# Optimization experiments

Measured on AMD Instinct MI355X. Metric: run time of the kernel, lower is better.

The kernel has to match this reference:

```python
import jax, jax.numpy as jnp
import numpy as np

B, S, D = 8, 4096, 512
H, DH = 8, 64  # heads, dim_head; inner_dim = H*DH = 512
EPS = 1e-6


def setup_inputs() -> dict:
    key = jax.random.key(0)
    ks = jax.random.split(key, 9)
    scale = 1.0 / np.sqrt(D)
    inner = H * DH
    return {
        "x": jax.random.normal(ks[0], (B, S, D), dtype=jnp.float32),
        "Wq": jax.random.normal(ks[1], (D, inner), dtype=jnp.float32) * scale,
        "bq": jax.random.normal(ks[2], (inner,), dtype=jnp.float32) * 0.01,
        "Wk": jax.random.normal(ks[3], (D, inner), dtype=jnp.float32) * scale,
        "bk": jax.random.normal(ks[4], (inner,), dtype=jnp.float32) * 0.01,
        "Wv": jax.random.normal(ks[5], (D, inner), dtype=jnp.float32) * scale,
        "bv": jax.random.normal(ks[6], (inner,), dtype=jnp.float32) * 0.01,
        "Wo": jax.random.normal(ks[7], (inner, D), dtype=jnp.float32) * (1.0 / np.sqrt(inner)),
        "bo": jax.random.normal(ks[8], (D,), dtype=jnp.float32) * 0.01,
    }


def _phi(x):
    # elu(x) + 1, the fast-transformers default feature map
    return jax.nn.elu(x) + 1.0


def reference(x, Wq, bq, Wk, bk, Wv, bv, Wo, bo):
    b, s, _ = x.shape
    q = (x @ Wq + bq).reshape(b, s, H, DH)
    k = (x @ Wk + bk).reshape(b, s, H, DH)
    v = (x @ Wv + bv).reshape(b, s, H, DH)

    Qf = _phi(q)  # [b, s, h, d]
    Kf = _phi(k)  # [b, s, h, d]

    # KV = sum_s Kf_s (outer) v_s  -> [b, h, d, m]
    KV = jnp.einsum('bshd,bshm->bhdm', Kf, v)
    # normalizer: Z = 1 / (Qf . sum_s Kf + eps)  -> [b, s, h]
    Ksum = Kf.sum(axis=1)  # [b, h, d]
    Z = 1.0 / (jnp.einsum('bshd,bhd->bsh', Qf, Ksum) + EPS)
    out = jnp.einsum('bshd,bhdm,bsh->bshm', Qf, KV, Z)  # [b, s, h, m]

    out = out.reshape(b, s, H * DH)
    return out @ Wo + bo  # dropout is identity at inference
```

## Files before the change

kernel.cpp:

```cpp
#include <hip/hip_runtime.h>
#include <hip/hip_fp16.h>


constexpr int Ss = 4096;
constexpr int Dd = 512;
constexpr int Hh = 8;
constexpr int Mtot = 8 * 4096;
constexpr float EPSF = 1e-6f;

typedef short v8s __attribute__((ext_vector_type(8)));
typedef float v4f __attribute__((ext_vector_type(4)));

__device__ __forceinline__ short f2bf(float f) {
  unsigned u = __float_as_uint(f);
  u += 0x7fff + ((u >> 16) & 1);
  return (short)(u >> 16);
}
__device__ __forceinline__ float bf2f(short s) {
  return __uint_as_float(((unsigned)(unsigned short)s) << 16);
}
__device__ __forceinline__ void async_cp16(const void* g, void* l) {
  __builtin_amdgcn_global_load_lds((__attribute__((address_space(1))) void*)g,
                                   (__attribute__((address_space(3))) void*)l, 16, 0, 0);
}

__global__ __launch_bounds__(256) void prep_w(
    const float* __restrict__ W0, const float* __restrict__ W1,
    const float* __restrict__ W2, const float* __restrict__ W3,
    short* __restrict__ Th, short* __restrict__ Tl)
{
  const float* W = (blockIdx.z == 0) ? W0 : (blockIdx.z == 1) ? W1
                  : (blockIdx.z == 2) ? W2 : W3;
  short* th = Th + (size_t)blockIdx.z * 512 * 512;
  short* tl = Tl + (size_t)blockIdx.z * 512 * 512;
  __shared__ float tile[32][33];
  const int t = threadIdx.x;
  const int tx = t & 31, ty = t >> 5;
  const int k0 = blockIdx.x * 32, n0 = blockIdx.y * 32;
#pragma unroll
  for (int r = 0; r < 32; r += 8)
    tile[ty + r][tx] = W[(size_t)(k0 + ty + r) * 512 + n0 + tx];
  __syncthreads();
#pragma unroll
  for (int r = 0; r < 32; r += 8) {
    const float v = tile[tx][ty + r];
    const short h = f2bf(v);
    const short l = f2bf(v - bf2f(h));
    th[(size_t)(n0 + ty + r) * 512 + k0 + tx] = h;
    tl[(size_t)(n0 + ty + r) * 512 + k0 + tx] = l;
  }
}

__global__ __launch_bounds__(256) void split_x(
    const float* __restrict__ X, short* __restrict__ H, short* __restrict__ L, int n4)
{
  const int i = blockIdx.x * 256 + threadIdx.x;
  if (i >= n4) return;
  const float4 x = reinterpret_cast<const float4*>(X)[i];
  short4 h, l;
  h.x = f2bf(x.x); l.x = f2bf(x.x - bf2f(h.x));
  h.y = f2bf(x.y); l.y = f2bf(x.y - bf2f(h.y));
  h.z = f2bf(x.z); l.z = f2bf(x.z - bf2f(h.z));
  h.w = f2bf(x.w); l.w = f2bf(x.w - bf2f(h.w));
  reinterpret_cast<short4*>(H)[i] = h;
  reinterpret_cast<short4*>(L)[i] = l;
}

__device__ __forceinline__ void stage_tile(
    const short* __restrict__ pA, const short* __restrict__ pB,
    short* as, short* bs, int k0, int t)
{
#pragma unroll
  for (int c = 0; c < 2; ++c) {
    const int idx = t + c * 512;
    const int row = idx >> 2;
    const int q = (idx & 3) ^ ((row >> 1) & 3);
    const size_t g = (size_t)row * 512 + k0 + q * 8;
    async_cp16(pA + g, as + idx * 8);
    async_cp16(pB + g, bs + idx * 8);
  }
}

__global__ __launch_bounds__(512, 2) void gemm_qkv(
    const short* __restrict__ Ah, const short* __restrict__ Al,
    const short* __restrict__ Wth, const short* __restrict__ Wtl,
    const float* __restrict__ bq, const float* __restrict__ bk,
    const float* __restrict__ bv,
    __half* __restrict__ Qf, __half* __restrict__ Kf, __half* __restrict__ Vv)
{
  __shared__ short As[2][256 * 32];
  __shared__ short Bs[2][256 * 32];

  const int mat = blockIdx.y >> 1;
  const int col0 = (blockIdx.y & 1) * 256;
  const int row0 = blockIdx.x * 256;
  const float* bias = (mat == 0) ? bq : (mat == 1) ? bk : bv;
  __half* Co = (mat == 0) ? Qf : (mat == 1) ? Kf : Vv;
  const int act = (mat < 2);

  const short* Ahb = Ah + (size_t)row0 * 512;
  const short* Alb = Al + (size_t)row0 * 512;
  const short* Bhb = Wth + (size_t)mat * 512 * 512 + (size_t)col0 * 512;
  const short* Blb = Wtl + (size_t)mat * 512 * 512 + (size_t)col0 * 512;

  const int t = threadIdx.x;
  const int lane = t & 63;
  const int wv = t >> 6;
  const int wm = wv >> 2, wn = wv & 3;
  const int mr = lane & 15, kq = lane >> 4;

  int a_off[8], b_off[4];
#pragma unroll
  for (int i = 0; i < 8; ++i) {
    const int ma = wm * 128 + i * 16 + mr;
    a_off[i] = ma * 32 + (kq ^ ((ma >> 1) & 3)) * 8;
  }
#pragma unroll
  for (int j = 0; j < 4; ++j) {
    const int nb = wn * 64 + j * 16 + mr;
    b_off[j] = nb * 32 + (kq ^ ((nb >> 1) & 3)) * 8;
  }

  v4f acc[8][4];
#pragma unroll
  for (int i = 0; i < 8; ++i)
#pragma unroll
    for (int j = 0; j < 4; ++j) acc[i][j] = (v4f){0.f, 0.f, 0.f, 0.f};

  stage_tile(Ahb, Bhb, As[0], Bs[0], 0, t);

  for (int kt = 0; kt < 48; ++kt) {
    const int cur = kt & 1;
    if (kt + 1 < 48) {
      const int nx = kt + 1;
      const int pass = nx >> 4;
      const short* pA = (pass == 2) ? Alb : Ahb;
      const short* pB = (pass == 1) ? Blb : Bhb;
      stage_tile(pA, pB, As[cur ^ 1], Bs[cur ^ 1], (nx & 15) * 32, t);
      asm volatile("s_waitcnt vmcnt(4)" ::: "memory");
    } else {
      asm volatile("s_waitcnt vmcnt(0)" ::: "memory");
    }
    __builtin_amdgcn_s_barrier();
    asm volatile("" ::: "memory");

    v8s fb[4];
#pragma unroll
    for (int j = 0; j < 4; ++j)
      fb[j] = *reinterpret_cast<const v8s*>(&Bs[cur][b_off[j]]);
    __builtin_amdgcn_s_setprio(1);
#pragma unroll
    for (int i = 0; i < 8; ++i) {
      const v8s fa = *reinterpret_cast<const v8s*>(&As[cur][a_off[i]]);
#pragma unroll
      for (int j = 0; j < 4; ++j)
        acc[i][j] = __builtin_amdgcn_mfma_f32_16x16x32_bf16(fa, fb[j], acc[i][j], 0, 0, 0);
    }
    __builtin_amdgcn_s_setprio(0);
    asm volatile("" ::: "memory");
    __builtin_amdgcn_s_barrier();
  }

#pragma unroll
  for (int j = 0; j < 4; ++j) {
    const int nc = col0 + wn * 64 + j * 16 + mr;
    const float bz = bias[nc];
#pragma unroll
    for (int i = 0; i < 8; ++i) {
      const int mbase = row0 + wm * 128 + i * 16 + kq * 4;
#pragma unroll
      for (int r = 0; r < 4; ++r) {
        float v = acc[i][j][r] + bz;
        if (act) v = (v > 0.f) ? (v + 1.f) : __expf(v);
        Co[(size_t)(mbase + r) * 512 + nc] = __float2half(v);
      }
    }
  }
}

__global__ __launch_bounds__(512, 2) void gemm_split(
    const short* __restrict__ Ah, const short* __restrict__ Al,
    const short* __restrict__ Bh, const short* __restrict__ Bl,
    const float* __restrict__ bias, float* __restrict__ Cf)
{
  __shared__ short As[2][256 * 32];
  __shared__ short Bs[2][256 * 32];

  const int col0 = blockIdx.y * 256;
  const int row0 = blockIdx.x * 256;

  const short* Ahb = Ah + (size_t)row0 * 512;
  const short* Alb = Al + (size_t)row0 * 512;
  const short* Bhb = Bh + (size_t)col0 * 512;
  const short* Blb = Bl + (size_t)col0 * 512;

  const int t = threadIdx.x;
  const int lane = t & 63;
  const int wv = t >> 6;
  const int wm = wv >> 2, wn = wv & 3;
  const int mr = lane & 15, kq = lane >> 4;

  int a_off[8], b_off[4];
#pragma unroll
  for (int i = 0; i < 8; ++i) {
    const int ma = wm * 128 + i * 16 + mr;
    a_off[i] = ma * 32 + (kq ^ ((ma >> 1) & 3)) * 8;
  }
#pragma unroll
  for (int j = 0; j < 4; ++j) {
    const int nb = wn * 64 + j * 16 + mr;
    b_off[j] = nb * 32 + (kq ^ ((nb >> 1) & 3)) * 8;
  }

  v4f acc[8][4];
#pragma unroll
  for (int i = 0; i < 8; ++i)
#pragma unroll
    for (int j = 0; j < 4; ++j) acc[i][j] = (v4f){0.f, 0.f, 0.f, 0.f};

  stage_tile(Ahb, Bhb, As[0], Bs[0], 0, t);

  for (int kt = 0; kt < 48; ++kt) {
    const int cur = kt & 1;
    if (kt + 1 < 48) {
      const int nx = kt + 1;
      const int pass = nx >> 4;
      const short* pA = (pass == 2) ? Alb : Ahb;
      const short* pB = (pass == 1) ? Blb : Bhb;
      stage_tile(pA, pB, As[cur ^ 1], Bs[cur ^ 1], (nx & 15) * 32, t);
      asm volatile("s_waitcnt vmcnt(4)" ::: "memory");
    } else {
      asm volatile("s_waitcnt vmcnt(0)" ::: "memory");
    }
    __builtin_amdgcn_s_barrier();
    asm volatile("" ::: "memory");

    v8s fb[4];
#pragma unroll
    for (int j = 0; j < 4; ++j)
      fb[j] = *reinterpret_cast<const v8s*>(&Bs[cur][b_off[j]]);
    __builtin_amdgcn_s_setprio(1);
#pragma unroll
    for (int i = 0; i < 8; ++i) {
      const v8s fa = *reinterpret_cast<const v8s*>(&As[cur][a_off[i]]);
#pragma unroll
      for (int j = 0; j < 4; ++j)
        acc[i][j] = __builtin_amdgcn_mfma_f32_16x16x32_bf16(fa, fb[j], acc[i][j], 0, 0, 0);
    }
    __builtin_amdgcn_s_setprio(0);
    asm volatile("" ::: "memory");
    __builtin_amdgcn_s_barrier();
  }

#pragma unroll
  for (int j = 0; j < 4; ++j) {
    const int nc = col0 + wn * 64 + j * 16 + mr;
    const float bz = bias[nc];
#pragma unroll
    for (int i = 0; i < 8; ++i) {
      const int mbase = row0 + wm * 128 + i * 16 + kq * 4;
#pragma unroll
      for (int r = 0; r < 4; ++r) Cf[(size_t)(mbase + r) * 512 + nc] = acc[i][j][r] + bz;
    }
  }
}

__global__ __launch_bounds__(256) void kv_stage1(
    const __half* __restrict__ Kf, const __half* __restrict__ V,
    float* __restrict__ KVp, float* __restrict__ Ksp)
{
  const int sc = blockIdx.x, bh = blockIdx.y;
  const int b = bh >> 3, h = bh & 7;
  __shared__ float Ks[64][68];
  __shared__ float Vs[64][68];
  const int tid = threadIdx.x;
  const int dx = (tid >> 4) * 4;
  const int mx = (tid & 15) * 4;
  float acc[4][4];
#pragma unroll
  for (int i = 0; i < 4; ++i)
#pragma unroll
    for (int j = 0; j < 4; ++j) acc[i][j] = 0.f;
  float ksum_acc = 0.f;
  const size_t base = (size_t)b * Ss * Dd + (size_t)h * 64;

  for (int s0 = sc * 256; s0 < sc * 256 + 256; s0 += 64) {
#pragma unroll
    for (int l = 0; l < 2; ++l) {
      const int idx = tid + l * 256;
      const int rr = idx >> 3, cq = idx & 7;
      const size_t g = base + (size_t)(s0 + rr) * Dd + cq * 8;
      const __half2* k2 = reinterpret_cast<const __half2*>(Kf + g);
      const __half2* v2 = reinterpret_cast<const __half2*>(V + g);
#pragma unroll
      for (int u = 0; u < 4; ++u) {
        const float2 kf = __half22float2(k2[u]);
        const float2 vf = __half22float2(v2[u]);
        Ks[rr][cq * 8 + u * 2] = kf.x; Ks[rr][cq * 8 + u * 2 + 1] = kf.y;
        Vs[rr][cq * 8 + u * 2] = vf.x; Vs[rr][cq * 8 + u * 2 + 1] = vf.y;
      }
    }
    __syncthreads();
#pragma unroll 4
    for (int s = 0; s < 64; ++s) {
      const float4 kd = *reinterpret_cast<const float4*>(&Ks[s][dx]);
      const float4 vm = *reinterpret_cast<const float4*>(&Vs[s][mx]);
      const float ka[4] = {kd.x, kd.y, kd.z, kd.w};
      const float va[4] = {vm.x, vm.y, vm.z, vm.w};
#pragma unroll
      for (int i = 0; i < 4; ++i)
#pragma unroll
        for (int j = 0; j < 4; ++j) acc[i][j] = fmaf(ka[i], va[j], acc[i][j]);
    }
    if (tid < 64) {
#pragma unroll 8
      for (int s = 0; s < 64; ++s) ksum_acc += Ks[s][tid];
    }
    __syncthreads();
  }

  const size_t pb = (size_t)(sc * 64 + bh);
#pragma unroll
  for (int i = 0; i < 4; ++i) {
    const float4 ov = {acc[i][0], acc[i][1], acc[i][2], acc[i][3]};
    *reinterpret_cast<float4*>(&KVp[(pb * 64 + dx + i) * 64 + mx]) = ov;
  }
  if (tid < 64) Ksp[pb * 64 + tid] = ksum_acc;
}

__global__ __launch_bounds__(256) void kv_stage2(
    const float* __restrict__ KVp, const float* __restrict__ Ksp,
    float* __restrict__ KV, float* __restrict__ Ksum)
{
  const int bh = blockIdx.x, t = threadIdx.x;
  for (int e = t; e < 4096; e += 256) {
    float s = 0.f;
#pragma unroll
    for (int sc = 0; sc < 16; ++sc) s += KVp[((size_t)(sc * 64 + bh) << 12) + e];
    KV[(size_t)bh * 4096 + e] = s;
  }
  if (t < 64) {
    float s = 0.f;
#pragma unroll
    for (int sc = 0; sc < 16; ++sc) s += Ksp[(size_t)(sc * 64 + bh) * 64 + t];
    Ksum[bh * 64 + t] = s;
  }
}

__global__ __launch_bounds__(256) void attn_combine(
    const __half* __restrict__ Qf, const float* __restrict__ KV,
    const float* __restrict__ Ksum, short* __restrict__ Oh, short* __restrict__ Ol)
{
  const int h = blockIdx.y;
  const int r0 = blockIdx.x * 64;
  const int b = r0 >> 12;
  const int bh = b * Hh + h;
  __shared__ float Qs[64][68];
  __shared__ float KVs[64][68];
  __shared__ float Ksums[64];
  __shared__ float Zs[64];
  const int tid = threadIdx.x;

#pragma unroll
  for (int l = 0; l < 2; ++l) {
    const int idx = tid + l * 256;
    const int rr = idx >> 3, cq = idx & 7;
    const __half2* q2 = reinterpret_cast<const __half2*>(
        Qf + (size_t)(r0 + rr) * Dd + h * 64 + cq * 8);
#pragma unroll
    for (int u = 0; u < 4; ++u) {
      const float2 qf = __half22float2(q2[u]);
      Qs[rr][cq * 8 + u * 2] = qf.x; Qs[rr][cq * 8 + u * 2 + 1] = qf.y;
    }
  }
#pragma unroll
  for (int l = 0; l < 4; ++l) {
    const int idx = tid + l * 256;
    const int rr = idx >> 4, cq = idx & 15;
    *reinterpret_cast<float4*>(&KVs[rr][cq * 4]) = *reinterpret_cast<const float4*>(
        &KV[(size_t)bh * 4096 + rr * 64 + cq * 4]);
  }
  if (tid < 64) Ksums[tid] = Ksum[bh * 64 + tid];
  __syncthreads();

  if (tid < 64) {
    float z = 0.f;
#pragma unroll 8
    for (int d = 0; d < 64; ++d) z = fmaf(Qs[tid][d], Ksums[d], z);
    Zs[tid] = 1.f / (z + EPSF);
  }
  __syncthreads();

  const int rx = (tid >> 4) * 4, mx = (tid & 15) * 4;
  float acc[4][4];
#pragma unroll
  for (int i = 0; i < 4; ++i)
#pragma unroll
    for (int j = 0; j < 4; ++j) acc[i][j] = 0.f;

#pragma unroll 4
  for (int d = 0; d < 64; ++d) {
    const float4 vm = *reinterpret_cast<const float4*>(&KVs[d][mx]);
    const float va[4] = {vm.x, vm.y, vm.z, vm.w};
#pragma unroll
    for (int i = 0; i < 4; ++i) {
      const float q = Qs[rx + i][d];
#pragma unroll
      for (int j = 0; j < 4; ++j) acc[i][j] = fmaf(q, va[j], acc[i][j]);
    }
  }

#pragma unroll
  for (int i = 0; i < 4; ++i) {
    const float z = Zs[rx + i];
    short4 hv, lv;
    float o;
    o = acc[i][0] * z; hv.x = f2bf(o); lv.x = f2bf(o - bf2f(hv.x));
    o = acc[i][1] * z; hv.y = f2bf(o); lv.y = f2bf(o - bf2f(hv.y));
    o = acc[i][2] * z; hv.z = f2bf(o); lv.z = f2bf(o - bf2f(hv.z));
    o = acc[i][3] * z; hv.w = f2bf(o); lv.w = f2bf(o - bf2f(hv.w));
    const size_t off = (size_t)(r0 + rx + i) * Dd + h * 64 + mx;
    *reinterpret_cast<short4*>(&Oh[off]) = hv;
    *reinterpret_cast<short4*>(&Ol[off]) = lv;
  }
}

extern "C" void kernel_launch(void* const* d_in, const int* in_sizes, int n_in,
                              void* d_out, int out_size, void* d_ws, size_t ws_size,
                              hipStream_t stream) {
  const float* x  = (const float*)d_in[0];
  const float* Wq = (const float*)d_in[1];
  const float* bq = (const float*)d_in[2];
  const float* Wk = (const float*)d_in[3];
  const float* bk = (const float*)d_in[4];
  const float* Wv = (const float*)d_in[5];
  const float* bv = (const float*)d_in[6];
  const float* Wo = (const float*)d_in[7];
  const float* bo = (const float*)d_in[8];
  float* out = (float*)d_out;

  char* ws = (char*)d_ws;
  const size_t MB = (size_t)1 << 20;
  short*  x_hi  = (short*)(ws);
  short*  x_lo  = (short*)(ws + 32 * MB);
  short*  Wt_hi = (short*)(ws + 64 * MB);
  short*  Wt_lo = (short*)(ws + 66 * MB);
  __half* Qf    = (__half*)(ws + 68 * MB);
  __half* Kf    = (__half*)(ws + 100 * MB);
  __half* Vv    = (__half*)(ws + 132 * MB);
  float*  KVp   = (float*)(ws + 164 * MB);
  float*  Ksp   = (float*)(ws + 181 * MB);
  float*  KV    = (float*)(ws + 182 * MB);
  float*  Ksum  = (float*)(ws + 183 * MB);
  short*  attn_hi = x_hi;
  short*  attn_lo = x_lo;
  const size_t WSTEP = (size_t)512 * 512;

  prep_w<<<dim3(16, 16, 4), 256, 0, stream>>>(Wq, Wk, Wv, Wo, Wt_hi, Wt_lo);
  split_x<<<Mtot * Dd / 4 / 256, 256, 0, stream>>>(x, x_hi, x_lo, Mtot * Dd / 4);

  gemm_qkv<<<dim3(Mtot / 256, 6), 512, 0, stream>>>(
      x_hi, x_lo, Wt_hi, Wt_lo, bq, bk, bv, Qf, Kf, Vv);

  kv_stage1<<<dim3(16, 64), 256, 0, stream>>>(Kf, Vv, KVp, Ksp);
  kv_stage2<<<64, 256, 0, stream>>>(KVp, Ksp, KV, Ksum);
  attn_combine<<<dim3(Mtot / 64, Hh), 256, 0, stream>>>(Qf, KV, Ksum, attn_hi, attn_lo);

  gemm_split<<<dim3(Mtot / 256, 2), 512, 0, stream>>>(
      attn_hi, attn_lo, Wt_hi + 3 * WSTEP, Wt_lo + 3 * WSTEP, bo, out);
}
```

Before: 497.9 us.

## Restructure split-bf16 GEMM k-loop into 64-wide tiles with interleaved chunk prefetch

Replaces the per-iteration 32-wide K tile loop in both GEMM kernels with a shared helper that processes 64-wide K tiles (24 iterations instead of 48). Global-to-LDS loads for the next tile are split into four chunks issued between MFMA phases, spreading memory traffic across the compute. The aim is fewer barrier/waitcnt round trips per unit of MFMA work and better overlap of loads with matrix math. It doubles LDS use per block (64 KB), which may limit occupancy at 2 blocks per CU, and adds more barriers inside each iteration.

```diff
diff --git a/kernel.cpp b/kernel.cpp
--- a/kernel.cpp
+++ b/kernel.cpp
@@ -66,18 +66,123 @@
   reinterpret_cast<short4*>(L)[i] = l;
 }
 
-__device__ __forceinline__ void stage_tile(
+__device__ __forceinline__ void stage_chunk(
     const short* __restrict__ pA, const short* __restrict__ pB,
-    short* as, short* bs, int k0, int t)
-{
-#pragma unroll
-  for (int c = 0; c < 2; ++c) {
-    const int idx = t + c * 512;
-    const int row = idx >> 2;
-    const int q = (idx & 3) ^ ((row >> 1) & 3);
-    const size_t g = (size_t)row * 512 + k0 + q * 8;
-    async_cp16(pA + g, as + idx * 8);
-    async_cp16(pB + g, bs + idx * 8);
+    short* asub, short* bsub, int kb, int rh, int t)
+{
+  const int row = rh * 128 + (t >> 2);
+  const int q = t & 3;
+  const int qs = q ^ ((row >> 1) & 3);
+  const size_t g = (size_t)row * 512 + kb + qs * 8;
+  const int d = rh * 4096 + t * 8;
+  async_cp16(pA + g, asub + d);
+  async_cp16(pB + g, bsub + d);
+}
+
+__device__ __forceinline__ void kloop_8ph(
+    const short* __restrict__ Ahb, const short* __restrict__ Alb,
+    const short* __restrict__ Bhb, const short* __restrict__ Blb,
+    short* asb, short* bsb,
+    int wm, int wn, int mr, int kq, int t,
+    v4f (&acc)[8][4])
+{
+  constexpr int NT = 24;
+#pragma unroll
+  for (int i = 0; i < 8; ++i)
+#pragma unroll
+    for (int j = 0; j < 4; ++j) acc[i][j] = (v4f){0.f, 0.f, 0.f, 0.f};
+
+  int a_off[8], b_off[4];
+#pragma unroll
+  for (int i = 0; i < 8; ++i) {
+    const int ma = wm * 128 + i * 16 + mr;
+    a_off[i] = ma * 32 + (kq ^ ((ma >> 1) & 3)) * 8;
+  }
+#pragma unroll
+  for (int j = 0; j < 4; ++j) {
+    const int nb = wn * 64 + j * 16 + mr;
+    b_off[j] = nb * 32 + (kq ^ ((nb >> 1) & 3)) * 8;
+  }
+
+#pragma unroll
+  for (int c = 0; c < 4; ++c)
+    stage_chunk(Ahb, Bhb, asb + (c & 1) * 8192, bsb + (c & 1) * 8192,
+                (c & 1) * 32, c >> 1, t);
+
+  for (int kt = 0; kt < NT; ++kt) {
+    const int cur = kt & 1;
+    const short* as0 = asb + cur * 16384;
+    const short* as1 = as0 + 8192;
+    const short* bs0 = bsb + cur * 16384;
+    const short* bs1 = bs0 + 8192;
+    short* An = asb + (cur ^ 1) * 16384;
+    short* Bn = bsb + (cur ^ 1) * 16384;
+    const int nx = kt + 1;
+    const int pass = nx >> 3;
+    const short* pA = (pass == 2) ? Alb : Ahb;
+    const short* pB = (pass == 1) ? Blb : Bhb;
+    const int kb = (nx & 7) * 64;
+
+    if (nx < NT) {
+      stage_chunk(pA, pB, An, Bn, kb, 0, t);
+      asm volatile("s_waitcnt vmcnt(2)" ::: "memory");
+    } else {
+      asm volatile("s_waitcnt vmcnt(0)" ::: "memory");
+    }
+    __builtin_amdgcn_s_barrier();
+    asm volatile("" ::: "memory");
+
+    v8s fb[4][2];
+#pragma unroll
+    for (int j = 0; j < 4; ++j) {
+      fb[j][0] = *reinterpret_cast<const v8s*>(&bs0[b_off[j]]);
+      fb[j][1] = *reinterpret_cast<const v8s*>(&bs1[b_off[j]]);
+    }
+    {
+      const v8s fa00 = *reinterpret_cast<const v8s*>(&as0[a_off[0]]);
+      const v8s fa01 = *reinterpret_cast<const v8s*>(&as1[a_off[0]]);
+      const v8s fa10 = *reinterpret_cast<const v8s*>(&as0[a_off[1]]);
+      const v8s fa11 = *reinterpret_cast<const v8s*>(&as1[a_off[1]]);
+      __builtin_amdgcn_s_setprio(1);
+#pragma unroll
+      for (int j = 0; j < 4; ++j) {
+        acc[0][j] = __builtin_amdgcn_mfma_f32_16x16x32_bf16(fa00, fb[j][0], acc[0][j], 0, 0, 0);
+        acc[0][j] = __builtin_amdgcn_mfma_f32_16x16x32_bf16(fa01, fb[j][1], acc[0][j], 0, 0, 0);
+        acc[1][j] = __builtin_amdgcn_mfma_f32_16x16x32_bf16(fa10, fb[j][0], acc[1][j], 0, 0, 0);
+        acc[1][j] = __builtin_amdgcn_mfma_f32_16x16x32_bf16(fa11, fb[j][1], acc[1][j], 0, 0, 0);
+      }
+      __builtin_amdgcn_s_setprio(0);
+    }
+    asm volatile("" ::: "memory");
+    __builtin_amdgcn_s_barrier();
+
+#pragma unroll
+    for (int p = 1; p < 4; ++p) {
+      const v8s fa00 = *reinterpret_cast<const v8s*>(&as0[a_off[2 * p]]);
+      const v8s fa01 = *reinterpret_cast<const v8s*>(&as1[a_off[2 * p]]);
+      const v8s fa10 = *reinterpret_cast<const v8s*>(&as0[a_off[2 * p + 1]]);
+      const v8s fa11 = *reinterpret_cast<const v8s*>(&as1[a_off[2 * p + 1]]);
+      if (nx < NT)
+        stage_chunk(pA, pB, An + (p & 1) * 8192, Bn + (p & 1) * 8192,
+                    kb + (p & 1) * 32, p >> 1, t);
+      __builtin_amdgcn_s_barrier();
+      asm volatile("" ::: "memory");
+      __builtin_amdgcn_s_setprio(1);
+#pragma unroll
+      for (int j = 0; j < 4; ++j) {
+        acc[2 * p][j] =
+            __builtin_amdgcn_mfma_f32_16x16x32_bf16(fa00, fb[j][0], acc[2 * p][j], 0, 0, 0);
+        acc[2 * p][j] =
+            __builtin_amdgcn_mfma_f32_16x16x32_bf16(fa01, fb[j][1], acc[2 * p][j], 0, 0, 0);
+        acc[2 * p + 1][j] =
+            __builtin_amdgcn_mfma_f32_16x16x32_bf16(fa10, fb[j][0], acc[2 * p + 1][j], 0, 0, 0);
+        acc[2 * p + 1][j] =
+            __builtin_amdgcn_mfma_f32_16x16x32_bf16(fa11, fb[j][1], acc[2 * p + 1][j], 0, 0, 0);
+      }
+      __builtin_amdgcn_s_setprio(0);
+      asm volatile("" ::: "memory");
+      __builtin_amdgcn_s_barrier();
+    }
   }
 }
 
@@ -88,8 +193,8 @@
     const float* __restrict__ bv,
     __half* __restrict__ Qf, __half* __restrict__ Kf, __half* __restrict__ Vv)
 {
-  __shared__ short As[2][256 * 32];
-  __shared__ short Bs[2][256 * 32];
+  __shared__ __align__(16) short As[2][2][8192];
+  __shared__ __align__(16) short Bs[2][2][8192];
 
   const int mat = blockIdx.y >> 1;
   const int col0 = (blockIdx.y & 1) * 256;
@@ -109,57 +214,8 @@
   const int wm = wv >> 2, wn = wv & 3;
   const int mr = lane & 15, kq = lane >> 4;
 
-  int a_off[8], b_off[4];
-#pragma unroll
-  for (int i = 0; i < 8; ++i) {
-    const int ma = wm * 128 + i * 16 + mr;
-    a_off[i] = ma * 32 + (kq ^ ((ma >> 1) & 3)) * 8;
-  }
-#pragma unroll
-  for (int j = 0; j < 4; ++j) {
-    const int nb = wn * 64 + j * 16 + mr;
-    b_off[j] = nb * 32 + (kq ^ ((nb >> 1) & 3)) * 8;
-  }
-
   v4f acc[8][4];
-#pragma unroll
-  for (int i = 0; i < 8; ++i)
-#pragma unroll
-    for (int j = 0; j < 4; ++j) acc[i][j] = (v4f){0.f, 0.f, 0.f, 0.f};
-
-  stage_tile(Ahb, Bhb, As[0], Bs[0], 0, t);
-
-  for (int kt = 0; kt < 48; ++kt) {
-    const int cur = kt & 1;
-    if (kt + 1 < 48) {
-      const int nx = kt + 1;
-      const int pass = nx >> 4;
-      const short* pA = (pass == 2) ? Alb : Ahb;
-      const short* pB = (pass == 1) ? Blb : Bhb;
-      stage_tile(pA, pB, As[cur ^ 1], Bs[cur ^ 1], (nx & 15) * 32, t);
-      asm volatile("s_waitcnt vmcnt(4)" ::: "memory");
-    } else {
-      asm volatile("s_waitcnt vmcnt(0)" ::: "memory");
-    }
-    __builtin_amdgcn_s_barrier();
-    asm volatile("" ::: "memory");
-
-    v8s fb[4];
-#pragma unroll
-    for (int j = 0; j < 4; ++j)
-      fb[j] = *reinterpret_cast<const v8s*>(&Bs[cur][b_off[j]]);
-    __builtin_amdgcn_s_setprio(1);
-#pragma unroll
-    for (int i = 0; i < 8; ++i) {
-      const v8s fa = *reinterpret_cast<const v8s*>(&As[cur][a_off[i]]);
-#pragma unroll
-      for (int j = 0; j < 4; ++j)
-        acc[i][j] = __builtin_amdgcn_mfma_f32_16x16x32_bf16(fa, fb[j], acc[i][j], 0, 0, 0);
-    }
-    __builtin_amdgcn_s_setprio(0);
-    asm volatile("" ::: "memory");
-    __builtin_amdgcn_s_barrier();
-  }
+  kloop_8ph(Ahb, Alb, Bhb, Blb, &As[0][0][0], &Bs[0][0][0], wm, wn, mr, kq, t, acc);
 
 #pragma unroll
   for (int j = 0; j < 4; ++j) {
@@ -183,8 +239,8 @@
     const short* __restrict__ Bh, const short* __restrict__ Bl,
     const float* __restrict__ bias, float* __restrict__ Cf)
 {
-  __shared__ short As[2][256 * 32];
-  __shared__ short Bs[2][256 * 32];
+  __shared__ __align__(16) short As[2][2][8192];
+  __shared__ __align__(16) short Bs[2][2][8192];
 
   const int col0 = blockIdx.y * 256;
   const int row0 = blockIdx.x * 256;
@@ -200,57 +256,8 @@
   const int wm = wv >> 2, wn = wv & 3;
   const int mr = lane & 15, kq = lane >> 4;
 
-  int a_off[8], b_off[4];
-#pragma unroll
-  for (int i = 0; i < 8; ++i) {
-    const int ma = wm * 128 + i * 16 + mr;
-    a_off[i] = ma * 32 + (kq ^ ((ma >> 1) & 3)) * 8;
-  }
-#pragma unroll
-  for (int j = 0; j < 4; ++j) {
-    const int nb = wn * 64 + j * 16 + mr;
-    b_off[j] = nb * 32 + (kq ^ ((nb >> 1) & 3)) * 8;
-  }
-
   v4f acc[8][4];
-#pragma unroll
-  for (int i = 0; i < 8; ++i)
-#pragma unroll
-    for (int j = 0; j < 4; ++j) acc[i][j] = (v4f){0.f, 0.f, 0.f, 0.f};
-
-  stage_tile(Ahb, Bhb, As[0], Bs[0], 0, t);
-
-  for (int kt = 0; kt < 48; ++kt) {
-    const int cur = kt & 1;
-    if (kt + 1 < 48) {
-      const int nx = kt + 1;
-      const int pass = nx >> 4;
-      const short* pA = (pass == 2) ? Alb : Ahb;
-      const short* pB = (pass == 1) ? Blb : Bhb;
-      stage_tile(pA, pB, As[cur ^ 1], Bs[cur ^ 1], (nx & 15) * 32, t);
-      asm volatile("s_waitcnt vmcnt(4)" ::: "memory");
-    } else {
-      asm volatile("s_waitcnt vmcnt(0)" ::: "memory");
-    }
-    __builtin_amdgcn_s_barrier();
-    asm volatile("" ::: "memory");
-
-    v8s fb[4];
-#pragma unroll
-    for (int j = 0; j < 4; ++j)
-      fb[j] = *reinterpret_cast<const v8s*>(&Bs[cur][b_off[j]]);
-    __builtin_amdgcn_s_setprio(1);
-#pragma unroll
-    for (int i = 0; i < 8; ++i) {
-      const v8s fa = *reinterpret_cast<const v8s*>(&As[cur][a_off[i]]);
-#pragma unroll
-      for (int j = 0; j < 4; ++j)
-        acc[i][j] = __builtin_amdgcn_mfma_f32_16x16x32_bf16(fa, fb[j], acc[i][j], 0, 0, 0);
-    }
-    __builtin_amdgcn_s_setprio(0);
-    asm volatile("" ::: "memory");
-    __builtin_amdgcn_s_barrier();
-  }
+  kloop_8ph(Ahb, Alb, Bhb, Blb, &As[0][0][0], &Bs[0][0][0], wm, wn, mr, kq, t, acc);
 
 #pragma unroll
   for (int j = 0; j < 4; ++j) {
```

Measured after the change: 466.5 us. 6.3% less time.
